# Kernel optimization log

Measured on AMD Instinct MI355X. Metric: run time of the kernel, lower is better.

Reference implementation:

```python
import jax, jax.numpy as jnp
import numpy as np

N, T, D, H = 256, 64, 1024, 1024


def setup_inputs() -> dict:
    key = jax.random.key(0)
    k1, k2, k3, k4, k5 = jax.random.split(key, 5)
    x = jax.random.normal(k1, (N, T, D), dtype=jnp.float32)
    A = jax.random.normal(k2, (N, H, 4, 4), dtype=jnp.float32)
    Wx = jax.random.normal(k3, (D, 4 * H), dtype=jnp.float32) / np.sqrt(D)
    Wh = jax.random.normal(k4, (H, 4 * H), dtype=jnp.float32) / np.sqrt(H)
    Wattn = jax.random.normal(k5, (H, 4 * H), dtype=jnp.float32) / np.sqrt(H)
    b = jnp.zeros((4 * H,), dtype=jnp.float32)
    return {"x": x, "A": A, "Wx": Wx, "Wh": Wh, "Wattn": Wattn, "b": b}


def reference(x, A, Wx, Wh, Wattn, b):
    n, t, d = x.shape
    h_dim = A.shape[1]
    L = A.shape[2] * A.shape[3]  # 16 spatial locations
    A_flat = A.reshape(n, h_dim, L)  # (N, H, 16)
    scale = 1.0 / (h_dim ** 0.5)
    h0 = A_flat.mean(axis=2)  # global mean-pooled feature, (N, H)
    c0 = h0

    def step(carry, xt):
        h, c = carry
        # scaled dot-product attention over 4x4 grid
        w = jax.nn.softmax(jnp.einsum('nh,nhl->nl', h, A_flat) * scale, axis=1)
        attn = jnp.einsum('nhl,nl->nh', A_flat, w)
        a = h @ Wh + xt @ Wx + attn @ Wattn + b  # (N, 4H)
        a_i, a_f, a_o, a_g = jnp.split(a, 4, axis=1)
        i = jax.nn.sigmoid(a_i)
        f = jax.nn.sigmoid(a_f)
        o = jax.nn.sigmoid(a_o)
        g = jnp.tanh(a_g)
        c_next = f * c + i * g
        h_next = o * jnp.tanh(c_next)
        return (h_next, c_next), h_next

    xs = jnp.swapaxes(x, 0, 1)  # (T, N, D)
    _, hs = jax.lax.scan(step, (h0, c0), xs)
    return jnp.swapaxes(hs, 0, 1)  # (N, T, H)
```

## Files before the change

### kernel.cpp

```cpp
#include <hip/hip_runtime.h>
#include <math.h>

#define NB 256
#define TT 64
#define DD 1024
#define HH 1024

typedef __attribute__((ext_vector_type(8))) short short8;
typedef __attribute__((ext_vector_type(4))) float floatx4;

__device__ inline unsigned short f2bf(float f) {
    unsigned int u = __builtin_bit_cast(unsigned int, f);
    u += 0x7fffu + ((u >> 16) & 1u);
    return (unsigned short)(u >> 16);
}
__device__ inline float bf2f(unsigned int h16) {
    unsigned int u = h16 << 16;
    return __builtin_bit_cast(float, u);
}

__device__ inline void async_copy16(const unsigned short* g, unsigned short* l) {
    __builtin_amdgcn_global_load_lds(
        (const __attribute__((address_space(1))) unsigned int*)(g),
        (__attribute__((address_space(3))) unsigned int*)(l), 16, 0, 0);
}

__global__ void k_convW(const float* __restrict__ Wh,
                        const float* __restrict__ Wattn,
                        const float* __restrict__ Wx,
                        unsigned short* __restrict__ Wsw) {
    int u = blockIdx.x * 256 + threadIdx.x;
    int tile = u >> 9;
    int nj = tile / 48, kc = tile % 48;
    int within = u & 511;
    int kq = within >> 6, cc = within & 63;
    int k = kc * 64 + kq * 8;
    int col = (cc >> 4) * 1024 + nj * 16 + (cc & 15);
    const float* src;
    if (k < 1024)       src = Wh    + (size_t)k * 4096 + col;
    else if (k < 2048)  src = Wattn + (size_t)(k - 1024) * 4096 + col;
    else                src = Wx    + (size_t)(k - 2048) * 4096 + col;
    unsigned int w[4];
#pragma unroll
    for (int j = 0; j < 4; ++j) {
        unsigned int lo = f2bf(src[(size_t)(2 * j) * 4096]);
        unsigned int hi = f2bf(src[(size_t)(2 * j + 1) * 4096]);
        w[j] = lo | (hi << 16);
    }
    ((uint4*)Wsw)[u] = make_uint4(w[0], w[1], w[2], w[3]);
}

__global__ __launch_bounds__(256) void k_convX(const float* __restrict__ x,
                                               unsigned short* __restrict__ xF) {
    const int t  = blockIdx.x >> 4;
    const int mb = blockIdx.x & 15;
    const int tid = threadIdx.x;
    __shared__ unsigned short xb[16][1032];

#pragma unroll
    for (int mm = 0; mm < 16; ++mm) {
        int m = mb * 16 + mm;
        const float4* src = (const float4*)(x + (size_t)m * (TT * DD) + (size_t)t * DD);
        float4 v = src[tid];
        unsigned int w0 = f2bf(v.x) | (f2bf(v.y) << 16);
        unsigned int w1 = f2bf(v.z) | (f2bf(v.w) << 16);
        *(uint2*)&xb[mm][tid * 4] = make_uint2(w0, w1);
    }
    __syncthreads();

#pragma unroll
    for (int i = 0; i < 8; ++i) {
        int u = i * 256 + tid;
        int kq = u >> 4, mm = u & 15;
        uint4 val = *(const uint4*)&xb[mm][kq * 8];
        size_t gu = (size_t)t * 32768 + (size_t)kq * 256 + mb * 16 + mm;
        ((uint4*)xF)[gu] = val;
    }
}

__global__ void k_convA_init(const float* __restrict__ A,
                             unsigned short* __restrict__ Abf,
                             float* __restrict__ h0,
                             float* __restrict__ c) {
    int idx = blockIdx.x * 256 + threadIdx.x;
    const float4* ap = (const float4*)(A + (size_t)idx * 16);
    float4 v0 = ap[0], v1 = ap[1], v2 = ap[2], v3 = ap[3];
    float vs[16] = {v0.x, v0.y, v0.z, v0.w, v1.x, v1.y, v1.z, v1.w,
                    v2.x, v2.y, v2.z, v2.w, v3.x, v3.y, v3.z, v3.w};
    float s = 0.f;
    unsigned int w[8];
#pragma unroll
    for (int j = 0; j < 8; ++j) {
        s += vs[2 * j] + vs[2 * j + 1];
        w[j] = f2bf(vs[2 * j]) | (f2bf(vs[2 * j + 1]) << 16);
    }
    ((uint4*)Abf)[idx * 2]     = make_uint4(w[0], w[1], w[2], w[3]);
    ((uint4*)Abf)[idx * 2 + 1] = make_uint4(w[4], w[5], w[6], w[7]);
    s *= (1.f / 16.f);
    h0[idx] = s;
    c[idx] = s;
}

__global__ __launch_bounds__(256) void k_attn(
    const unsigned short* __restrict__ Abf,
    const float* __restrict__ hprev, int hstride,
    unsigned short* __restrict__ lhsF) {
    const int n = blockIdx.x;
    const int tid = threadIdx.x;
    const int lane = tid & 63, wave = tid >> 6;

    float4 hv = *(const float4*)(hprev + (size_t)n * hstride + tid * 4);
    const uint4* ar = (const uint4*)(Abf + ((size_t)n * 1024 + tid * 4) * 16);

    float a[4][16];
#pragma unroll
    for (int r = 0; r < 4; ++r) {
        uint4 p0 = ar[r * 2], p1 = ar[r * 2 + 1];
        unsigned int ws[8] = {p0.x, p0.y, p0.z, p0.w, p1.x, p1.y, p1.z, p1.w};
#pragma unroll
        for (int j = 0; j < 8; ++j) {
            a[r][2 * j]     = bf2f(ws[j] & 0xffffu);
            a[r][2 * j + 1] = bf2f(ws[j] >> 16);
        }
    }
    float hvv[4] = {hv.x, hv.y, hv.z, hv.w};
    float s[16];
#pragma unroll
    for (int l = 0; l < 16; ++l) {
        float t = 0.f;
#pragma unroll
        for (int r = 0; r < 4; ++r) t += hvv[r] * a[r][l];
        s[l] = t;
    }

#pragma unroll
    for (int off = 32; off > 0; off >>= 1) {
#pragma unroll
        for (int l = 0; l < 16; ++l) s[l] += __shfl_xor(s[l], off, 64);
    }
    __shared__ float wred[4 * 16];
    if (lane == 0) {
#pragma unroll
        for (int l = 0; l < 16; ++l) wred[wave * 16 + l] = s[l];
    }
    __syncthreads();

    const float scale = 0.03125f;
    float sv[16];
#pragma unroll
    for (int l = 0; l < 16; ++l)
        sv[l] = (wred[l] + wred[16 + l] + wred[32 + l] + wred[48 + l]) * scale;
    float mx = sv[0];
#pragma unroll
    for (int l = 1; l < 16; ++l) mx = fmaxf(mx, sv[l]);
    float e[16], sum = 0.f;
#pragma unroll
    for (int l = 0; l < 16; ++l) { e[l] = __expf(sv[l] - mx); sum += e[l]; }
    float inv = 1.f / sum;
#pragma unroll
    for (int l = 0; l < 16; ++l) e[l] *= inv;

    unsigned short hb[4], ab[4];
#pragma unroll
    for (int r = 0; r < 4; ++r) {
        float acc = 0.f;
#pragma unroll
        for (int l = 0; l < 16; ++l) acc += a[r][l] * e[l];
        ab[r] = f2bf(acc);
        hb[r] = f2bf(hvv[r]);
    }
    unsigned int hw0 = (unsigned int)hb[0] | ((unsigned int)hb[1] << 16);
    unsigned int hw1 = (unsigned int)hb[2] | ((unsigned int)hb[3] << 16);
    unsigned int aw0 = (unsigned int)ab[0] | ((unsigned int)ab[1] << 16);
    unsigned int aw1 = (unsigned int)ab[2] | ((unsigned int)ab[3] << 16);
    size_t hu = ((size_t)(tid >> 1) * 256 + n) * 8 + (size_t)(tid & 1) * 4;
    size_t au = ((size_t)(128 + (tid >> 1)) * 256 + n) * 8 + (size_t)(tid & 1) * 4;
    *(uint2*)(lhsF + hu) = make_uint2(hw0, hw1);
    *(uint2*)(lhsF + au) = make_uint2(aw0, aw1);
}

__global__ __launch_bounds__(256) void k_step(
    const unsigned short* __restrict__ lhsF,
    const unsigned short* __restrict__ xFt,
    const unsigned short* __restrict__ Wsw,
    const float* __restrict__ b,
    float* __restrict__ c,
    float* __restrict__ out_t) {
    const int nj = blockIdx.x, mi = blockIdx.y;
    const int tid = threadIdx.x;
    const int lane = tid & 63, wave = tid >> 6;
    const int wm = wave & 1, wn = wave >> 1;
    const int l15 = lane & 15, quad = lane >> 4;
    const int waveBase = tid & ~63;

    __shared__ __align__(16) unsigned short lds[8 * 8192];

    floatx4 acc[2][2];
#pragma unroll
    for (int mt = 0; mt < 2; ++mt)
#pragma unroll
        for (int nt = 0; nt < 2; ++nt) acc[mt][nt] = (floatx4)0.f;

    const unsigned short* wTile = Wsw + (size_t)nj * (48 * 512 * 8);

    auto stage = [&](int kc, int buf) {
        unsigned short* la = lds + (size_t)buf * 8192;
        unsigned short* lb = la + 4096;
        const unsigned short* as_ = (kc < 32)
            ? lhsF + ((size_t)(kc * 8) * 256 + (size_t)mi * 64) * 8
            : xFt + ((size_t)((kc - 32) * 8) * 256 + (size_t)mi * 64) * 8;
#pragma unroll
        for (int i = 0; i < 2; ++i) {
            int idx = i * 256 + tid;
            int kq = idx >> 6, mm = idx & 63;
            async_copy16(as_ + ((size_t)kq * 256 + mm) * 8,
                         la + (size_t)(i * 256 + waveBase) * 8);
        }
        const unsigned short* bs = wTile + (size_t)kc * 512 * 8;
#pragma unroll
        for (int i = 0; i < 2; ++i) {
            int idx = i * 256 + tid;
            async_copy16(bs + (size_t)idx * 8,
                         lb + (size_t)(i * 256 + waveBase) * 8);
        }
    };

    auto compute = [&](int buf) {
        const unsigned short* la = lds + (size_t)buf * 8192;
        const unsigned short* lb = la + 4096;
#pragma unroll
        for (int ks = 0; ks < 2; ++ks) {
            const int kqq = ks * 4 + quad;
            short8 af[2], bfr[2];
#pragma unroll
            for (int mt = 0; mt < 2; ++mt)
                af[mt] = *(const short8*)(la + (size_t)(kqq * 64 + wm * 32 + mt * 16 + l15) * 8);
#pragma unroll
            for (int nt = 0; nt < 2; ++nt)
                bfr[nt] = *(const short8*)(lb + (size_t)(kqq * 64 + wn * 32 + nt * 16 + l15) * 8);
#pragma unroll
            for (int mt = 0; mt < 2; ++mt)
#pragma unroll
                for (int nt = 0; nt < 2; ++nt)
                    acc[mt][nt] = __builtin_amdgcn_mfma_f32_16x16x32_bf16(
                        af[mt], bfr[nt], acc[mt][nt], 0, 0, 0);
        }
    };

    stage(0, 0);
    stage(1, 1);
    stage(2, 2);
    stage(3, 3);
    stage(4, 4);
    stage(5, 5);

#pragma unroll 4
    for (int kc = 0; kc < 42; ++kc) {
        asm volatile("s_waitcnt vmcnt(20)\n\ts_barrier" ::: "memory");
        stage(kc + 6, (kc + 6) & 7);
        compute(kc & 7);
    }
    asm volatile("s_waitcnt vmcnt(20)\n\ts_barrier" ::: "memory");
    compute(42 & 7);
    asm volatile("s_waitcnt vmcnt(16)\n\ts_barrier" ::: "memory");
    compute(43 & 7);
    asm volatile("s_waitcnt vmcnt(12)\n\ts_barrier" ::: "memory");
    compute(44 & 7);
    asm volatile("s_waitcnt vmcnt(8)\n\ts_barrier" ::: "memory");
    compute(45 & 7);
    asm volatile("s_waitcnt vmcnt(4)\n\ts_barrier" ::: "memory");
    compute(46 & 7);
    asm volatile("s_waitcnt vmcnt(0)\n\ts_barrier" ::: "memory");
    compute(47 & 7);

    __syncthreads();
    float* asF = (float*)lds;
#pragma unroll
    for (int mt = 0; mt < 2; ++mt)
#pragma unroll
        for (int nt = 0; nt < 2; ++nt)
#pragma unroll
            for (int r = 0; r < 4; ++r) {
                int row = wm * 32 + mt * 16 + quad * 4 + r;
                int cc = wn * 32 + nt * 16 + l15;
                asF[row * 64 + cc] = acc[mt][nt][r];
            }
    __syncthreads();

    const int j15 = tid & 15;
    const int jj = nj * 16 + j15;
    const float bi = b[jj], bf_ = b[1024 + jj], bo = b[2048 + jj], bg = b[3072 + jj];
#pragma unroll
    for (int i = 0; i < 4; ++i) {
        int cell = i * 256 + tid;
        int row = cell >> 4;
        float ai  = asF[row * 64 + j15]      + bi;
        float af2 = asF[row * 64 + 16 + j15] + bf_;
        float ao  = asF[row * 64 + 32 + j15] + bo;
        float ag  = asF[row * 64 + 48 + j15] + bg;
        float iv = 1.f / (1.f + __expf(-ai));
        float fv = 1.f / (1.f + __expf(-af2));
        float ov = 1.f / (1.f + __expf(-ao));
        float gv = 1.f - 2.f / (__expf(2.f * ag) + 1.f);
        int n = mi * 64 + row;
        size_t ci = (size_t)n * HH + jj;
        float cold = c[ci];
        float cn = fv * cold + iv * gv;
        c[ci] = cn;
        float th = 1.f - 2.f / (__expf(2.f * cn) + 1.f);
        out_t[(size_t)n * (TT * HH) + jj] = ov * th;
    }
}

extern "C" void kernel_launch(void* const* d_in, const int* in_sizes, int n_in,
                              void* d_out, int out_size, void* d_ws, size_t ws_size,
                              hipStream_t stream) {
    const float* x     = (const float*)d_in[0];
    const float* A     = (const float*)d_in[1];
    const float* Wx    = (const float*)d_in[2];
    const float* Wh    = (const float*)d_in[3];
    const float* Wattn = (const float*)d_in[4];
    const float* b     = (const float*)d_in[5];
    float* out = (float*)d_out;

    char* w = (char*)d_ws;
    unsigned short* Wsw  = (unsigned short*)(w);
    unsigned short* xF   = (unsigned short*)(w + 25165824);
    unsigned short* lhsF = (unsigned short*)(w + 58720256);
    unsigned short* Abf  = (unsigned short*)(w + 59768832);
    float* h0            = (float*)(w + 68157440);
    float* c             = (float*)(w + 69206016);

    k_convW<<<6144, 256, 0, stream>>>(Wh, Wattn, Wx, Wsw);
    k_convX<<<1024, 256, 0, stream>>>(x, xF);
    k_convA_init<<<1024, 256, 0, stream>>>(A, Abf, h0, c);

    for (int t = 0; t < TT; ++t) {
        const float* hprev = (t == 0) ? h0 : out + (size_t)(t - 1) * HH;
        int hstride = (t == 0) ? HH : TT * HH;
        k_attn<<<NB, 256, 0, stream>>>(Abf, hprev, hstride, lhsF);
        k_step<<<dim3(64, 4), 256, 0, stream>>>(
            lhsF, xF + (size_t)t * 262144, Wsw, b, c, out + (size_t)t * HH);
    }
}
```

Before: 1.370 ms.

## Hoist input projection x@Wx out of recurrence into one batched GEMM

Adds a k_xw kernel that computes x_t@Wx for all 64 timesteps in one large parallel GEMM up front and stores the result as bf16. The per-step k_step kernel then only runs the K=2048 recurrent part (h and attn) instead of K=3072, and adds the precomputed x projection in its epilogue. The LDS ring buffer shrinks from 8 to 4 stages. This shortens the serial critical path and gives the x projection much better occupancy, at the cost of a large workspace buffer, extra bf16 rounding of the x contribution, and per-step reads of that buffer.

```diff
diff --git a/kernel.cpp b/kernel.cpp
--- a/kernel.cpp
+++ b/kernel.cpp
@@ -101,6 +101,102 @@
     c[idx] = s;
 }
 
+__global__ __launch_bounds__(256) void k_xw(
+    const unsigned short* __restrict__ xF,
+    const unsigned short* __restrict__ Wsw,
+    unsigned short* __restrict__ xw) {
+    const int nj = blockIdx.x, mi = blockIdx.y, t = blockIdx.z;
+    const int tid = threadIdx.x;
+    const int lane = tid & 63, wave = tid >> 6;
+    const int wm = wave & 1, wn = wave >> 1;
+    const int l15 = lane & 15, quad = lane >> 4;
+    const int waveBase = tid & ~63;
+
+    __shared__ __align__(16) unsigned short lds[4 * 8192];
+
+    floatx4 acc[2][2];
+#pragma unroll
+    for (int mt = 0; mt < 2; ++mt)
+#pragma unroll
+        for (int nt = 0; nt < 2; ++nt) acc[mt][nt] = (floatx4)0.f;
+
+    const unsigned short* wTile = Wsw + (size_t)nj * (48 * 512 * 8) + (size_t)32 * 4096;
+    const unsigned short* xSlab = xF + (size_t)t * 262144;
+
+    auto stage = [&](int kc, int buf) {
+        unsigned short* la = lds + (size_t)buf * 8192;
+        unsigned short* lb = la + 4096;
+        const unsigned short* as_ = xSlab + ((size_t)(kc * 8) * 256 + (size_t)mi * 64) * 8;
+#pragma unroll
+        for (int i = 0; i < 2; ++i) {
+            int idx = i * 256 + tid;
+            int kq = idx >> 6, mm = idx & 63;
+            async_copy16(as_ + ((size_t)kq * 256 + mm) * 8,
+                         la + (size_t)(i * 256 + waveBase) * 8);
+        }
+        const unsigned short* bs = wTile + (size_t)kc * 4096;
+#pragma unroll
+        for (int i = 0; i < 2; ++i) {
+            int idx = i * 256 + tid;
+            async_copy16(bs + (size_t)idx * 8,
+                         lb + (size_t)(i * 256 + waveBase) * 8);
+        }
+    };
+
+    auto compute = [&](int buf) {
+        const unsigned short* la = lds + (size_t)buf * 8192;
+        const unsigned short* lb = la + 4096;
+#pragma unroll
+        for (int ks = 0; ks < 2; ++ks) {
+            const int kqq = ks * 4 + quad;
+            short8 af[2], bfr[2];
+#pragma unroll
+            for (int mt = 0; mt < 2; ++mt)
+                af[mt] = *(const short8*)(la + (size_t)(kqq * 64 + wm * 32 + mt * 16 + l15) * 8);
+#pragma unroll
+            for (int nt = 0; nt < 2; ++nt)
+                bfr[nt] = *(const short8*)(lb + (size_t)(kqq * 64 + wn * 32 + nt * 16 + l15) * 8);
+#pragma unroll
+            for (int mt = 0; mt < 2; ++mt)
+#pragma unroll
+                for (int nt = 0; nt < 2; ++nt)
+                    acc[mt][nt] = __builtin_amdgcn_mfma_f32_16x16x32_bf16(
+                        af[mt], bfr[nt], acc[mt][nt], 0, 0, 0);
+        }
+    };
+
+    stage(0, 0);
+    stage(1, 1);
+    stage(2, 2);
+
+#pragma unroll 4
+    for (int kc = 0; kc < 13; ++kc) {
+        asm volatile("s_waitcnt vmcnt(8)\n\ts_barrier" ::: "memory");
+        stage(kc + 3, (kc + 3) & 3);
+        compute(kc & 3);
+    }
+    asm volatile("s_waitcnt vmcnt(8)\n\ts_barrier" ::: "memory");
+    compute(13 & 3);
+    asm volatile("s_waitcnt vmcnt(4)\n\ts_barrier" ::: "memory");
+    compute(14 & 3);
+    asm volatile("s_waitcnt vmcnt(0)\n\ts_barrier" ::: "memory");
+    compute(15 & 3);
+
+    size_t base = ((size_t)t * 256 + (size_t)mi * 64) * 4096;
+#pragma unroll
+    for (int mt = 0; mt < 2; ++mt)
+#pragma unroll
+        for (int nt = 0; nt < 2; ++nt)
+#pragma unroll
+            for (int r = 0; r < 4; ++r) {
+                int row = wm * 32 + mt * 16 + quad * 4 + r;
+                int ccc = wn * 32 + nt * 16 + l15;
+                int gcol = (ccc >> 4) * 1024 + nj * 16 + (ccc & 15);
+                __builtin_nontemporal_store(f2bf(acc[mt][nt][r]),
+                                            xw + base + (size_t)row * 4096 + gcol);
+            }
+}
+
 __global__ __launch_bounds__(256) void k_attn(
     const unsigned short* __restrict__ Abf,
     const float* __restrict__ hprev, int hstride,
@@ -181,10 +277,10 @@
 
 __global__ __launch_bounds__(256) void k_step(
     const unsigned short* __restrict__ lhsF,
-    const unsigned short* __restrict__ xFt,
     const unsigned short* __restrict__ Wsw,
     const float* __restrict__ b,
     float* __restrict__ c,
+    const unsigned short* __restrict__ xwt,
     float* __restrict__ out_t) {
     const int nj = blockIdx.x, mi = blockIdx.y;
     const int tid = threadIdx.x;
@@ -193,7 +289,7 @@
     const int l15 = lane & 15, quad = lane >> 4;
     const int waveBase = tid & ~63;
 
-    __shared__ __align__(16) unsigned short lds[8 * 8192];
+    __shared__ __align__(16) unsigned short lds[4 * 8192];
 
     floatx4 acc[2][2];
 #pragma unroll
@@ -206,9 +302,7 @@
     auto stage = [&](int kc, int buf) {
         unsigned short* la = lds + (size_t)buf * 8192;
         unsigned short* lb = la + 4096;
-        const unsigned short* as_ = (kc < 32)
-            ? lhsF + ((size_t)(kc * 8) * 256 + (size_t)mi * 64) * 8
-            : xFt + ((size_t)((kc - 32) * 8) * 256 + (size_t)mi * 64) * 8;
+        const unsigned short* as_ = lhsF + ((size_t)(kc * 8) * 256 + (size_t)mi * 64) * 8;
 #pragma unroll
         for (int i = 0; i < 2; ++i) {
             int idx = i * 256 + tid;
@@ -250,28 +344,19 @@
     stage(0, 0);
     stage(1, 1);
     stage(2, 2);
-    stage(3, 3);
-    stage(4, 4);
-    stage(5, 5);
 
 #pragma unroll 4
-    for (int kc = 0; kc < 42; ++kc) {
-        asm volatile("s_waitcnt vmcnt(20)\n\ts_barrier" ::: "memory");
-        stage(kc + 6, (kc + 6) & 7);
-        compute(kc & 7);
-    }
-    asm volatile("s_waitcnt vmcnt(20)\n\ts_barrier" ::: "memory");
-    compute(42 & 7);
-    asm volatile("s_waitcnt vmcnt(16)\n\ts_barrier" ::: "memory");
-    compute(43 & 7);
-    asm volatile("s_waitcnt vmcnt(12)\n\ts_barrier" ::: "memory");
-    compute(44 & 7);
+    for (int kc = 0; kc < 29; ++kc) {
+        asm volatile("s_waitcnt vmcnt(8)\n\ts_barrier" ::: "memory");
+        stage(kc + 3, (kc + 3) & 3);
+        compute(kc & 3);
+    }
     asm volatile("s_waitcnt vmcnt(8)\n\ts_barrier" ::: "memory");
-    compute(45 & 7);
+    compute(29 & 3);
     asm volatile("s_waitcnt vmcnt(4)\n\ts_barrier" ::: "memory");
-    compute(46 & 7);
+    compute(30 & 3);
     asm volatile("s_waitcnt vmcnt(0)\n\ts_barrier" ::: "memory");
-    compute(47 & 7);
+    compute(31 & 3);
 
     __syncthreads();
     float* asF = (float*)lds;
@@ -294,15 +379,20 @@
     for (int i = 0; i < 4; ++i) {
         int cell = i * 256 + tid;
         int row = cell >> 4;
-        float ai  = asF[row * 64 + j15]      + bi;
-        float af2 = asF[row * 64 + 16 + j15] + bf_;
-        float ao  = asF[row * 64 + 32 + j15] + bo;
-        float ag  = asF[row * 64 + 48 + j15] + bg;
+        int n = mi * 64 + row;
+        const unsigned short* xr = xwt + (size_t)n * 4096 + jj;
+        float xi = bf2f(__builtin_nontemporal_load(xr));
+        float xf = bf2f(__builtin_nontemporal_load(xr + 1024));
+        float xo = bf2f(__builtin_nontemporal_load(xr + 2048));
+        float xg = bf2f(__builtin_nontemporal_load(xr + 3072));
+        float ai  = asF[row * 64 + j15]      + bi + xi;
+        float af2 = asF[row * 64 + 16 + j15] + bf_ + xf;
+        float ao  = asF[row * 64 + 32 + j15] + bo + xo;
+        float ag  = asF[row * 64 + 48 + j15] + bg + xg;
         float iv = 1.f / (1.f + __expf(-ai));
         float fv = 1.f / (1.f + __expf(-af2));
         float ov = 1.f / (1.f + __expf(-ao));
         float gv = 1.f - 2.f / (__expf(2.f * ag) + 1.f);
-        int n = mi * 64 + row;
         size_t ci = (size_t)n * HH + jj;
         float cold = c[ci];
         float cn = fv * cold + iv * gv;
@@ -326,20 +416,22 @@
     char* w = (char*)d_ws;
     unsigned short* Wsw  = (unsigned short*)(w);
     unsigned short* xF   = (unsigned short*)(w + 25165824);
-    unsigned short* lhsF = (unsigned short*)(w + 58720256);
-    unsigned short* Abf  = (unsigned short*)(w + 59768832);
-    float* h0            = (float*)(w + 68157440);
-    float* c             = (float*)(w + 69206016);
+    unsigned short* xw   = (unsigned short*)(w + 58720256);
+    unsigned short* lhsF = (unsigned short*)(w + 192937984);
+    unsigned short* Abf  = (unsigned short*)(w + 193986560);
+    float* h0            = (float*)(w + 202375168);
+    float* c             = (float*)(w + 203423744);
 
     k_convW<<<6144, 256, 0, stream>>>(Wh, Wattn, Wx, Wsw);
     k_convX<<<1024, 256, 0, stream>>>(x, xF);
     k_convA_init<<<1024, 256, 0, stream>>>(A, Abf, h0, c);
+    k_xw<<<dim3(64, 4, 64), 256, 0, stream>>>(xF, Wsw, xw);
 
     for (int t = 0; t < TT; ++t) {
         const float* hprev = (t == 0) ? h0 : out + (size_t)(t - 1) * HH;
         int hstride = (t == 0) ? HH : TT * HH;
         k_attn<<<NB, 256, 0, stream>>>(Abf, hprev, hstride, lhsF);
         k_step<<<dim3(64, 4), 256, 0, stream>>>(
-            lhsF, xF + (size_t)t * 262144, Wsw, b, c, out + (size_t)t * HH);
-    }
-}
+            lhsF, Wsw, b, c, xw + (size_t)t * (256 * 4096), out + (size_t)t * HH);
+    }
+}
```

Result: slower. 1.520 ms (+11.0%).

## Load A operand directly into registers and stage only weights through LDS

Applied to the files above, without the earlier changes.

The per-step GEMM kernel no longer copies the activation (A) tile into shared memory. Each wave now loads its own A fragments from global memory straight into registers with a three-deep register ring, while the weight tile still goes to LDS asynchronously through a four-buffer ring instead of eight. The goal is to cut LDS traffic and footprint, which could allow higher occupancy and fewer LDS reads per MFMA. In exchange, A fragments that waves share are now fetched redundantly from global memory, more registers are used, the pipeline is shallower, and the hand-tuned vmcnt counts must correctly cover the mixed register and LDS loads.

```diff
diff --git a/kernel.cpp b/kernel.cpp
--- a/kernel.cpp
+++ b/kernel.cpp
@@ -193,7 +193,7 @@
     const int l15 = lane & 15, quad = lane >> 4;
     const int waveBase = tid & ~63;
 
-    __shared__ __align__(16) unsigned short lds[8 * 8192];
+    __shared__ __align__(16) unsigned short lds[4 * 4096];
 
     floatx4 acc[2][2];
 #pragma unroll
@@ -203,20 +203,23 @@
 
     const unsigned short* wTile = Wsw + (size_t)nj * (48 * 512 * 8);
 
-    auto stage = [&](int kc, int buf) {
-        unsigned short* la = lds + (size_t)buf * 8192;
-        unsigned short* lb = la + 4096;
-        const unsigned short* as_ = (kc < 32)
+    auto aBase = [&](int kc) -> const unsigned short* {
+        return (kc < 32)
             ? lhsF + ((size_t)(kc * 8) * 256 + (size_t)mi * 64) * 8
             : xFt + ((size_t)((kc - 32) * 8) * 256 + (size_t)mi * 64) * 8;
-#pragma unroll
-        for (int i = 0; i < 2; ++i) {
-            int idx = i * 256 + tid;
-            int kq = idx >> 6, mm = idx & 63;
-            async_copy16(as_ + ((size_t)kq * 256 + mm) * 8,
-                         la + (size_t)(i * 256 + waveBase) * 8);
-        }
-        const unsigned short* bs = wTile + (size_t)kc * 512 * 8;
+    };
+    auto loadA = [&](short8* Ar, int kc) {
+        const unsigned short* ab_ = aBase(kc);
+#pragma unroll
+        for (int mt = 0; mt < 2; ++mt)
+#pragma unroll
+            for (int ks = 0; ks < 2; ++ks)
+                Ar[mt * 2 + ks] = *(const short8*)(ab_ +
+                    (size_t)((ks * 4 + quad) * 256 + wm * 32 + mt * 16 + l15) * 8);
+    };
+    auto stageB = [&](int kc, int buf) {
+        unsigned short* lb = lds + (size_t)buf * 4096;
+        const unsigned short* bs = wTile + (size_t)kc * 4096;
 #pragma unroll
         for (int i = 0; i < 2; ++i) {
             int idx = i * 256 + tid;
@@ -224,17 +227,12 @@
                          lb + (size_t)(i * 256 + waveBase) * 8);
         }
     };
-
-    auto compute = [&](int buf) {
-        const unsigned short* la = lds + (size_t)buf * 8192;
-        const unsigned short* lb = la + 4096;
+    auto computeB = [&](int buf, const short8* Ar) {
+        const unsigned short* lb = lds + (size_t)buf * 4096;
 #pragma unroll
         for (int ks = 0; ks < 2; ++ks) {
             const int kqq = ks * 4 + quad;
-            short8 af[2], bfr[2];
-#pragma unroll
-            for (int mt = 0; mt < 2; ++mt)
-                af[mt] = *(const short8*)(la + (size_t)(kqq * 64 + wm * 32 + mt * 16 + l15) * 8);
+            short8 bfr[2];
 #pragma unroll
             for (int nt = 0; nt < 2; ++nt)
                 bfr[nt] = *(const short8*)(lb + (size_t)(kqq * 64 + wn * 32 + nt * 16 + l15) * 8);
@@ -243,35 +241,31 @@
 #pragma unroll
                 for (int nt = 0; nt < 2; ++nt)
                     acc[mt][nt] = __builtin_amdgcn_mfma_f32_16x16x32_bf16(
-                        af[mt], bfr[nt], acc[mt][nt], 0, 0, 0);
+                        Ar[mt * 2 + ks], bfr[nt], acc[mt][nt], 0, 0, 0);
         }
     };
 
-    stage(0, 0);
-    stage(1, 1);
-    stage(2, 2);
-    stage(3, 3);
-    stage(4, 4);
-    stage(5, 5);
-
-#pragma unroll 4
-    for (int kc = 0; kc < 42; ++kc) {
-        asm volatile("s_waitcnt vmcnt(20)\n\ts_barrier" ::: "memory");
-        stage(kc + 6, (kc + 6) & 7);
-        compute(kc & 7);
-    }
-    asm volatile("s_waitcnt vmcnt(20)\n\ts_barrier" ::: "memory");
-    compute(42 & 7);
-    asm volatile("s_waitcnt vmcnt(16)\n\ts_barrier" ::: "memory");
-    compute(43 & 7);
+    short8 Areg[3][4];
+    stageB(0, 0);
+    stageB(1, 1);
+    stageB(2, 2);
+    loadA(Areg[0], 0);
+    loadA(Areg[1], 1);
+
+#pragma unroll 3
+    for (int kc = 0; kc < 45; ++kc) {
+        asm volatile("s_waitcnt vmcnt(12)\n\ts_barrier" ::: "memory");
+        loadA(Areg[(kc + 2) % 3], kc + 2);
+        stageB(kc + 3, (kc + 3) & 3);
+        computeB(kc & 3, Areg[kc % 3]);
+    }
     asm volatile("s_waitcnt vmcnt(12)\n\ts_barrier" ::: "memory");
-    compute(44 & 7);
-    asm volatile("s_waitcnt vmcnt(8)\n\ts_barrier" ::: "memory");
-    compute(45 & 7);
+    loadA(Areg[2], 47);
+    computeB(45 & 3, Areg[0]);
+    asm volatile("s_waitcnt vmcnt(10)\n\ts_barrier" ::: "memory");
+    computeB(46 & 3, Areg[1]);
     asm volatile("s_waitcnt vmcnt(4)\n\ts_barrier" ::: "memory");
-    compute(46 & 7);
-    asm volatile("s_waitcnt vmcnt(0)\n\ts_barrier" ::: "memory");
-    compute(47 & 7);
+    computeB(47 & 3, Areg[2]);
 
     __syncthreads();
     float* asF = (float*)lds;
```

After: 1.760 ms. 1.29x slower.
